# Performance work log

Measured on AMD Instinct MI355X. Metric: run time of the kernel, lower is better.

Reference implementation:

```python
import jax, jax.numpy as jnp
import numpy as np

N = 131072
D = 512        # input_dim
H = 512        # hidden_dim
E = 10         # num_experts
INIT_STD_SCALE = 0.1


def _trunc_normal(key, shape, std):
    # approximate trunc_normal_(std=std) in [-2std, 2std]
    return jnp.clip(jax.random.normal(key, shape) * std, -2.0 * std, 2.0 * std).astype(jnp.float32)


def setup_inputs() -> dict:
    key = jax.random.key(0)
    ks = jax.random.split(key, 6)
    x = jax.random.normal(ks[0], (N, D), dtype=jnp.float32)
    # router (default nn.Linear init approximated with uniform)
    lim = 1.0 / np.sqrt(D)
    Wr = jax.random.uniform(ks[1], (E, D), minval=-lim, maxval=lim, dtype=jnp.float32)
    br = jnp.zeros((E,), dtype=jnp.float32)
    # experts: trunc_normal with std = 0.1 / sqrt(fan_in), zero bias
    W1 = _trunc_normal(ks[2], (E, D, H), INIT_STD_SCALE / np.sqrt(D))   # [E, D, H]
    b1 = jnp.zeros((E, H), dtype=jnp.float32)
    W2 = _trunc_normal(ks[3], (E, H, H), INIT_STD_SCALE / np.sqrt(H))   # [E, H, H]
    b2 = jnp.zeros((E, H), dtype=jnp.float32)
    return {"x": x, "Wr": Wr, "br": br, "W1": W1, "b1": b1, "W2": W2, "b2": b2}


def reference(x, Wr, br, W1, b1, W2, b2):
    # router in fp32 (autocast disabled in original)
    logits = x.astype(jnp.float32) @ Wr.T + br          # [N, E]
    expert_ids = jnp.argmax(logits, axis=1)              # [N]
    out = jnp.zeros((x.shape[0], W2.shape[-1]), dtype=x.dtype)
    # fixed small loop over experts; dropout is identity at inference
    for e in range(W1.shape[0]):
        h = jax.nn.relu(x @ W1[e] + b1[e])                # [N, H]
        o = h @ W2[e] + b2[e]                             # [N, H]
        out = jnp.where((expert_ids == e)[:, None], o, out)
    return out, expert_ids
```

## Files before the change

kernel.cpp:

```cpp
#include <hip/hip_runtime.h>

#define N_TOK 131072
#define DIM   512
#define HID   512
#define NEXP  10

using bf16x8 = __attribute__((ext_vector_type(8))) short;
using f32x4  = __attribute__((ext_vector_type(4))) float;

__device__ __forceinline__ ushort f2bf(float f) {
    union { float f; unsigned u; } v; v.f = f;
    unsigned u = v.u;
    return (ushort)((u + 0x7FFFu + ((u >> 16) & 1u)) >> 16);
}

#define GLOAD16(g, l) __builtin_amdgcn_global_load_lds( \
    (const __attribute__((address_space(1))) void*)(g),  \
    (__attribute__((address_space(3))) void*)(l), 16, 0, 0)

__global__ __launch_bounds__(256) void router_kernel(
    const float* __restrict__ x, const float* __restrict__ Wr,
    const float* __restrict__ br, int* __restrict__ eid,
    float* __restrict__ ids_out, int* __restrict__ counts)
{
    __shared__ float wr[NEXP][DIM];
    __shared__ int lcnt[NEXP];
    int tid = threadIdx.x;
    for (int i = tid; i < NEXP * DIM / 4; i += 256)
        ((float4*)wr)[i] = ((const float4*)Wr)[i];
    if (tid < NEXP) lcnt[tid] = 0;
    __syncthreads();

    int lane  = tid & 63;
    int wave  = tid >> 6;
    int gwave = blockIdx.x * 4 + wave;
    int nwav  = gridDim.x * 4;

    for (int t = gwave; t < N_TOK; t += nwav) {
        const float4* xr = (const float4*)(x + (size_t)t * DIM);
        float4 v0 = xr[lane * 2], v1 = xr[lane * 2 + 1];
        float xf[8] = {v0.x, v0.y, v0.z, v0.w, v1.x, v1.y, v1.z, v1.w};
        float dot[NEXP];
        #pragma unroll
        for (int e = 0; e < NEXP; ++e) {
            const float* wv = &wr[e][lane * 8];
            float s = 0.f;
            #pragma unroll
            for (int j = 0; j < 8; ++j) s = fmaf(xf[j], wv[j], s);
            dot[e] = s;
        }
        #pragma unroll
        for (int off = 32; off > 0; off >>= 1) {
            #pragma unroll
            for (int e = 0; e < NEXP; ++e) dot[e] += __shfl_xor(dot[e], off, 64);
        }
        if (lane == 0) {
            int best = 0; float bv = dot[0] + br[0];
            #pragma unroll
            for (int e = 1; e < NEXP; ++e) {
                float v = dot[e] + br[e];
                if (v > bv) { bv = v; best = e; }
            }
            eid[t] = best;
            ids_out[t] = (float)best;
            atomicAdd(&lcnt[best], 1);
        }
    }
    __syncthreads();
    if (tid < NEXP) atomicAdd(&counts[tid], lcnt[tid]);
}

__global__ void offsets_kernel(const int* __restrict__ counts,
                               int* __restrict__ offsets, int* __restrict__ toff)
{
    if (threadIdx.x == 0) {
        int acc = 0, ta = 0;
        for (int e = 0; e < NEXP; ++e) {
            offsets[e] = acc; toff[e] = ta;
            acc += counts[e]; ta += (counts[e] + 63) >> 6;
        }
        offsets[NEXP] = acc; toff[NEXP] = ta;
    }
}

__global__ __launch_bounds__(256) void scatter_kernel(
    const int* __restrict__ eid, const int* __restrict__ offsets,
    int* __restrict__ cursors, int* __restrict__ perm)
{
    __shared__ int lcnt[NEXP], lbase[NEXP];
    int tid = threadIdx.x;
    if (tid < NEXP) lcnt[tid] = 0;
    __syncthreads();
    int t = blockIdx.x * 256 + tid;
    int e = 0, lpos = 0;
    if (t < N_TOK) {
        e = eid[t];
        lpos = atomicAdd(&lcnt[e], 1);
    }
    __syncthreads();
    if (tid < NEXP) lbase[tid] = atomicAdd(&cursors[tid], lcnt[tid]);
    __syncthreads();
    if (t < N_TOK) perm[offsets[e] + lbase[e] + lpos] = t;
}

__global__ __launch_bounds__(256) void wconvert_kernel(
    const float* __restrict__ W1, const float* __restrict__ W2,
    short* __restrict__ W1bT, short* __restrict__ W2bT)
{
    int mat = blockIdx.z;
    const float* src = (mat < NEXP) ? W1 + (size_t)mat * 512 * 512
                                    : W2 + (size_t)(mat - NEXP) * 512 * 512;
    short* dst = (mat < NEXP) ? W1bT + (size_t)mat * 512 * 512
                              : W2bT + (size_t)(mat - NEXP) * 512 * 512;
    __shared__ float tile[64][65];
    int r0 = blockIdx.y * 64, c0 = blockIdx.x * 64;
    int tid = threadIdx.x;
    int tr = tid >> 4, tc4 = (tid & 15) * 4;
    #pragma unroll
    for (int i = 0; i < 4; ++i) {
        float4 v = *(const float4*)(src + (size_t)(r0 + i * 16 + tr) * 512 + c0 + tc4);
        tile[i * 16 + tr][tc4 + 0] = v.x; tile[i * 16 + tr][tc4 + 1] = v.y;
        tile[i * 16 + tr][tc4 + 2] = v.z; tile[i * 16 + tr][tc4 + 3] = v.w;
    }
    __syncthreads();
    #pragma unroll
    for (int i = 0; i < 4; ++i) {
        int cc = i * 16 + tr;
        ushort4 o;
        o.x = f2bf(tile[tc4 + 0][cc]); o.y = f2bf(tile[tc4 + 1][cc]);
        o.z = f2bf(tile[tc4 + 2][cc]); o.w = f2bf(tile[tc4 + 3][cc]);
        *(ushort4*)(dst + (size_t)(c0 + cc) * 512 + r0 + tc4) = o;
    }
}

template<int LAYER>
__global__ __launch_bounds__(256, 2) void expert_gemm(
    const float* __restrict__ x, const short* __restrict__ hA,
    const short* __restrict__ WT, const float* __restrict__ bias,
    const int* __restrict__ offsets, const int* __restrict__ toff,
    const int* __restrict__ perm,
    short* __restrict__ hOut, float* __restrict__ out)
{
    int g = blockIdx.x;
    if (g >= toff[NEXP]) return;
    int e = 0;
    #pragma unroll
    for (int k = 1; k < NEXP; ++k) e += (g >= toff[k]);
    int beg = offsets[e], cnt = offsets[e + 1] - beg;
    int m0 = (g - toff[e]) * 64;

    __shared__ int toks[64];
    __shared__ short Abuf[2][64 * 32];
    __shared__ short Bbuf[2][512 * 32];

    int tid = threadIdx.x, lane = tid & 63, w = tid >> 6;
    if (tid < 64) toks[tid] = perm[beg + min(m0 + tid, cnt - 1)];
    __syncthreads();

    int srow = tid >> 2;
    int skq  = tid & 3;
    const float* asrcF = nullptr;
    const short* asrcH = nullptr;
    if (LAYER == 1) asrcF = x + (size_t)toks[srow] * DIM + skq * 8;
    else            asrcH = hA + (size_t)(beg + min(m0 + srow, cnt - 1)) * HID + skq * 8;
    const short* bsrc = WT + (size_t)e * 512 * 512 + (size_t)srow * 512 + skq * 8;

    auto stage = [&](int t, int b) {
        float4 a0, a1;
        if (LAYER == 1) {
            a0 = *(const float4*)(asrcF + t * 32);
            a1 = *(const float4*)(asrcF + t * 32 + 4);
        } else {
            GLOAD16(asrcH + t * 32, (char*)&Abuf[b][0] + w * 1024);
        }
        const short* bs = bsrc + t * 32;
        char* bl = (char*)&Bbuf[b][0] + w * 1024;
        #pragma unroll
        for (int r = 0; r < 8; ++r)
            GLOAD16(bs + (size_t)r * 64 * 512, bl + r * 4096);
        if (LAYER == 1) {
            bf16x8 ap;
            ap[0] = (short)f2bf(a0.x); ap[1] = (short)f2bf(a0.y);
            ap[2] = (short)f2bf(a0.z); ap[3] = (short)f2bf(a0.w);
            ap[4] = (short)f2bf(a1.x); ap[5] = (short)f2bf(a1.y);
            ap[6] = (short)f2bf(a1.z); ap[7] = (short)f2bf(a1.w);
            *(bf16x8*)((char*)&Abuf[b][0] + srow * 64 + skq * 16) = ap;
        }
    };

    f32x4 acc[4][8];
    #pragma unroll
    for (int i = 0; i < 4; ++i)
        #pragma unroll
        for (int j = 0; j < 8; ++j) acc[i][j] = (f32x4){0.f, 0.f, 0.f, 0.f};

    int lrow = lane & 15;
    int lk   = (lane >> 4) * 8;

    auto compute = [&](int b) {
        const short* A = &Abuf[b][0];
        const short* B = &Bbuf[b][0];
        bf16x8 af[4], bfv[8];
        #pragma unroll
        for (int i = 0; i < 4; ++i)
            af[i] = *(const bf16x8*)(A + (i * 16 + lrow) * 32 + lk);
        #pragma unroll
        for (int j = 0; j < 8; ++j)
            bfv[j] = *(const bf16x8*)(B + (w * 128 + j * 16 + lrow) * 32 + lk);
        #pragma unroll
        for (int i = 0; i < 4; ++i)
            #pragma unroll
            for (int j = 0; j < 8; ++j)
                acc[i][j] = __builtin_amdgcn_mfma_f32_16x16x32_bf16(af[i], bfv[j], acc[i][j], 0, 0, 0);
    };

    stage(0, 0);
    __syncthreads();
    #pragma unroll 1
    for (int t = 0; t < 14; t += 2) {
        stage(t + 1, 1); compute(0); __syncthreads();
        stage(t + 2, 0); compute(1); __syncthreads();
    }
    stage(15, 1); compute(0); __syncthreads();
    compute(1);

    const float* be = bias + (size_t)e * 512;
    int colb = w * 128 + lrow;
    float bv[8];
    #pragma unroll
    for (int j = 0; j < 8; ++j) bv[j] = be[colb + j * 16];

    #pragma unroll
    for (int i = 0; i < 4; ++i) {
        #pragma unroll
        for (int q = 0; q < 4; ++q) {
            int rr = i * 16 + ((lane >> 4) << 2) + q;
            if (m0 + rr < cnt) {
                if (LAYER == 1) {
                    short* hp = hOut + (size_t)(beg + m0 + rr) * HID + colb;
                    #pragma unroll
                    for (int j = 0; j < 8; ++j) {
                        float v = acc[i][j][q] + bv[j];
                        hp[j * 16] = (short)f2bf(v > 0.f ? v : 0.f);
                    }
                } else {
                    float* op = out + (size_t)toks[rr] * HID + colb;
                    #pragma unroll
                    for (int j = 0; j < 8; ++j)
                        op[j * 16] = acc[i][j][q] + bv[j];
                }
            }
        }
    }
}

extern "C" void kernel_launch(void* const* d_in, const int* in_sizes, int n_in,
                              void* d_out, int out_size, void* d_ws, size_t ws_size,
                              hipStream_t stream)
{
    const float* x  = (const float*)d_in[0];
    const float* Wr = (const float*)d_in[1];
    const float* br = (const float*)d_in[2];
    const float* W1 = (const float*)d_in[3];
    const float* b1 = (const float*)d_in[4];
    const float* W2 = (const float*)d_in[5];
    const float* b2 = (const float*)d_in[6];

    float* out     = (float*)d_out;
    float* ids_out = out + (size_t)N_TOK * HID;

    char* ws     = (char*)d_ws;
    int* counts  = (int*)ws;
    int* offsets = counts + 16;
    int* toff    = counts + 32;
    int* cursors = counts + 48;
    int* eid     = (int*)(ws + 1024);
    int* perm    = eid + N_TOK;
    short* W1bT  = (short*)(ws + 1024 + (size_t)2 * N_TOK * 4);
    short* W2bT  = W1bT + (size_t)NEXP * 512 * 512;
    short* h     = W2bT + (size_t)NEXP * 512 * 512;

    hipMemsetAsync(d_ws, 0, 1024, stream);
    router_kernel<<<2048, 256, 0, stream>>>(x, Wr, br, eid, ids_out, counts);
    wconvert_kernel<<<dim3(8, 8, 2 * NEXP), 256, 0, stream>>>(W1, W2, W1bT, W2bT);
    offsets_kernel<<<1, 64, 0, stream>>>(counts, offsets, toff);
    scatter_kernel<<<512, 256, 0, stream>>>(eid, offsets, cursors, perm);

    int ntiles = (N_TOK + 63) / 64 + NEXP;
    expert_gemm<1><<<ntiles, 256, 0, stream>>>(x, nullptr, W1bT, b1, offsets, toff, perm, h, nullptr);
    expert_gemm<2><<<ntiles, 256, 0, stream>>>(nullptr, h, W2bT, b2, offsets, toff, perm, nullptr, out);
}
```

Baseline: 434.0 us.

## Retile expert GEMM to 128x256 tiles with 8 waves and N split

Changes the grouped expert GEMM from 64-token x 512-column tiles with 4 waves to 128-token x 256-column tiles with 8 waves arranged 2x4, launching two column blocks per token tile. Each wave now holds a 64x64 accumulator instead of 64x128, which lowers register pressure and targets higher occupancy (launch bounds 512,4). The A tile is reused across more columns per weight load, but the A operand (including the layer-1 fp32 gather and bf16 conversion) is now loaded twice, once per column block. Padding waste per expert also grows with the larger row tile.

```diff
diff --git a/kernel.cpp b/kernel.cpp
--- a/kernel.cpp
+++ b/kernel.cpp
@@ -1,4 +1,5 @@
 #include <hip/hip_runtime.h>
+#include <hip/hip_bf16.h>
 
 #define N_TOK 131072
 #define DIM   512
@@ -8,10 +9,10 @@
 using bf16x8 = __attribute__((ext_vector_type(8))) short;
 using f32x4  = __attribute__((ext_vector_type(4))) float;
 
-__device__ __forceinline__ ushort f2bf(float f) {
+__device__ __forceinline__ short f2bf(float f) {
     union { float f; unsigned u; } v; v.f = f;
     unsigned u = v.u;
-    return (ushort)((u + 0x7FFFu + ((u >> 16) & 1u)) >> 16);
+    return (short)((u + 0x7FFFu + ((u >> 16) & 1u)) >> 16);
 }
 
 #define GLOAD16(g, l) __builtin_amdgcn_global_load_lds( \
@@ -77,7 +78,7 @@
         int acc = 0, ta = 0;
         for (int e = 0; e < NEXP; ++e) {
             offsets[e] = acc; toff[e] = ta;
-            acc += counts[e]; ta += (counts[e] + 63) >> 6;
+            acc += counts[e]; ta += (counts[e] + 127) >> 7;
         }
         offsets[NEXP] = acc; toff[NEXP] = ta;
     }
@@ -127,14 +128,14 @@
     for (int i = 0; i < 4; ++i) {
         int cc = i * 16 + tr;
         ushort4 o;
-        o.x = f2bf(tile[tc4 + 0][cc]); o.y = f2bf(tile[tc4 + 1][cc]);
-        o.z = f2bf(tile[tc4 + 2][cc]); o.w = f2bf(tile[tc4 + 3][cc]);
+        o.x = (ushort)f2bf(tile[tc4 + 0][cc]); o.y = (ushort)f2bf(tile[tc4 + 1][cc]);
+        o.z = (ushort)f2bf(tile[tc4 + 2][cc]); o.w = (ushort)f2bf(tile[tc4 + 3][cc]);
         *(ushort4*)(dst + (size_t)(c0 + cc) * 512 + r0 + tc4) = o;
     }
 }
 
 template<int LAYER>
-__global__ __launch_bounds__(256, 2) void expert_gemm(
+__global__ __launch_bounds__(512, 4) void expert_gemm(
     const float* __restrict__ x, const short* __restrict__ hA,
     const short* __restrict__ WT, const float* __restrict__ bias,
     const int* __restrict__ offsets, const int* __restrict__ toff,
@@ -147,70 +148,65 @@
     #pragma unroll
     for (int k = 1; k < NEXP; ++k) e += (g >= toff[k]);
     int beg = offsets[e], cnt = offsets[e + 1] - beg;
-    int m0 = (g - toff[e]) * 64;
-
-    __shared__ int toks[64];
-    __shared__ short Abuf[2][64 * 32];
-    __shared__ short Bbuf[2][512 * 32];
+    int m0 = (g - toff[e]) * 128;
+    int nb = blockIdx.y * 256;
+
+    __shared__ int toks[128];
+    __shared__ short Abuf[2][128 * 32];
+    __shared__ short Bbuf[2][256 * 32];
 
     int tid = threadIdx.x, lane = tid & 63, w = tid >> 6;
-    if (tid < 64) toks[tid] = perm[beg + min(m0 + tid, cnt - 1)];
-    __syncthreads();
-
-    int srow = tid >> 2;
-    int skq  = tid & 3;
-    const float* asrcF = nullptr;
-    const short* asrcH = nullptr;
-    if (LAYER == 1) asrcF = x + (size_t)toks[srow] * DIM + skq * 8;
-    else            asrcH = hA + (size_t)(beg + min(m0 + srow, cnt - 1)) * HID + skq * 8;
-    const short* bsrc = WT + (size_t)e * 512 * 512 + (size_t)srow * 512 + skq * 8;
+    if (tid < 128) toks[tid] = perm[beg + min(m0 + tid, cnt - 1)];
+    __syncthreads();
+
+    int arow = tid >> 2;
+    int kq   = tid & 3;
+    const float* xr   = nullptr;
+    const short* ha   = nullptr;
+    if (LAYER == 1) xr = x + (size_t)toks[arow] * DIM + kq * 8;
+    else            ha = hA + (size_t)(beg + min(m0 + arow, cnt - 1)) * HID + kq * 8;
+    const short* bp = WT + (size_t)e * 512 * 512 + (size_t)(nb + (tid >> 2)) * 512 + kq * 8;
 
     auto stage = [&](int t, int b) {
-        float4 a0, a1;
+        char* bl = (char*)&Bbuf[b][0] + w * 1024;
+        GLOAD16(bp + t * 32,         bl);
+        GLOAD16(bp + t * 32 + 65536, bl + 8192);
         if (LAYER == 1) {
-            a0 = *(const float4*)(asrcF + t * 32);
-            a1 = *(const float4*)(asrcF + t * 32 + 4);
+            float4 a0 = *(const float4*)(xr + t * 32);
+            float4 a1 = *(const float4*)(xr + t * 32 + 4);
+            bf16x8 p;
+            p[0] = f2bf(a0.x); p[1] = f2bf(a0.y); p[2] = f2bf(a0.z); p[3] = f2bf(a0.w);
+            p[4] = f2bf(a1.x); p[5] = f2bf(a1.y); p[6] = f2bf(a1.z); p[7] = f2bf(a1.w);
+            *(bf16x8*)((char*)&Abuf[b][0] + tid * 16) = p;
         } else {
-            GLOAD16(asrcH + t * 32, (char*)&Abuf[b][0] + w * 1024);
-        }
-        const short* bs = bsrc + t * 32;
-        char* bl = (char*)&Bbuf[b][0] + w * 1024;
-        #pragma unroll
-        for (int r = 0; r < 8; ++r)
-            GLOAD16(bs + (size_t)r * 64 * 512, bl + r * 4096);
-        if (LAYER == 1) {
-            bf16x8 ap;
-            ap[0] = (short)f2bf(a0.x); ap[1] = (short)f2bf(a0.y);
-            ap[2] = (short)f2bf(a0.z); ap[3] = (short)f2bf(a0.w);
-            ap[4] = (short)f2bf(a1.x); ap[5] = (short)f2bf(a1.y);
-            ap[6] = (short)f2bf(a1.z); ap[7] = (short)f2bf(a1.w);
-            *(bf16x8*)((char*)&Abuf[b][0] + srow * 64 + skq * 16) = ap;
+            GLOAD16(ha + t * 32, (char*)&Abuf[b][0] + w * 1024);
         }
     };
 
-    f32x4 acc[4][8];
+    f32x4 acc[4][4];
     #pragma unroll
     for (int i = 0; i < 4; ++i)
         #pragma unroll
-        for (int j = 0; j < 8; ++j) acc[i][j] = (f32x4){0.f, 0.f, 0.f, 0.f};
-
+        for (int j = 0; j < 4; ++j) acc[i][j] = (f32x4){0.f, 0.f, 0.f, 0.f};
+
+    int wr = w >> 2, wc = w & 3;
     int lrow = lane & 15;
     int lk   = (lane >> 4) * 8;
 
     auto compute = [&](int b) {
         const short* A = &Abuf[b][0];
         const short* B = &Bbuf[b][0];
-        bf16x8 af[4], bfv[8];
+        bf16x8 af[4], bfv[4];
         #pragma unroll
         for (int i = 0; i < 4; ++i)
-            af[i] = *(const bf16x8*)(A + (i * 16 + lrow) * 32 + lk);
-        #pragma unroll
-        for (int j = 0; j < 8; ++j)
-            bfv[j] = *(const bf16x8*)(B + (w * 128 + j * 16 + lrow) * 32 + lk);
+            af[i] = *(const bf16x8*)(A + (wr * 64 + i * 16 + lrow) * 32 + lk);
+        #pragma unroll
+        for (int j = 0; j < 4; ++j)
+            bfv[j] = *(const bf16x8*)(B + (wc * 64 + j * 16 + lrow) * 32 + lk);
         #pragma unroll
         for (int i = 0; i < 4; ++i)
             #pragma unroll
-            for (int j = 0; j < 8; ++j)
+            for (int j = 0; j < 4; ++j)
                 acc[i][j] = __builtin_amdgcn_mfma_f32_16x16x32_bf16(af[i], bfv[j], acc[i][j], 0, 0, 0);
     };
 
@@ -225,28 +221,28 @@
     compute(1);
 
     const float* be = bias + (size_t)e * 512;
-    int colb = w * 128 + lrow;
-    float bv[8];
-    #pragma unroll
-    for (int j = 0; j < 8; ++j) bv[j] = be[colb + j * 16];
+    int colb = nb + wc * 64 + lrow;
+    float bv[4];
+    #pragma unroll
+    for (int j = 0; j < 4; ++j) bv[j] = be[colb + j * 16];
 
     #pragma unroll
     for (int i = 0; i < 4; ++i) {
         #pragma unroll
         for (int q = 0; q < 4; ++q) {
-            int rr = i * 16 + ((lane >> 4) << 2) + q;
+            int rr = wr * 64 + i * 16 + ((lane >> 4) << 2) + q;
             if (m0 + rr < cnt) {
                 if (LAYER == 1) {
                     short* hp = hOut + (size_t)(beg + m0 + rr) * HID + colb;
                     #pragma unroll
-                    for (int j = 0; j < 8; ++j) {
+                    for (int j = 0; j < 4; ++j) {
                         float v = acc[i][j][q] + bv[j];
-                        hp[j * 16] = (short)f2bf(v > 0.f ? v : 0.f);
+                        hp[j * 16] = f2bf(v > 0.f ? v : 0.f);
                     }
                 } else {
                     float* op = out + (size_t)toks[rr] * HID + colb;
                     #pragma unroll
-                    for (int j = 0; j < 8; ++j)
+                    for (int j = 0; j < 4; ++j)
                         op[j * 16] = acc[i][j][q] + bv[j];
                 }
             }
@@ -286,7 +282,7 @@
     offsets_kernel<<<1, 64, 0, stream>>>(counts, offsets, toff);
     scatter_kernel<<<512, 256, 0, stream>>>(eid, offsets, cursors, perm);
 
-    int ntiles = (N_TOK + 63) / 64 + NEXP;
-    expert_gemm<1><<<ntiles, 256, 0, stream>>>(x, nullptr, W1bT, b1, offsets, toff, perm, h, nullptr);
-    expert_gemm<2><<<ntiles, 256, 0, stream>>>(nullptr, h, W2bT, b2, offsets, toff, perm, nullptr, out);
-}
+    int ntiles = (N_TOK + 127) / 128 + NEXP;
+    expert_gemm<1><<<dim3(ntiles, 2), 512, 0, stream>>>(x, nullptr, W1bT, b1, offsets, toff, perm, h, nullptr);
+    expert_gemm<2><<<dim3(ntiles, 2), 512, 0, stream>>>(nullptr, h, W2bT, b2, offsets, toff, perm, nullptr, out);
+}
```

After: 434.4 us. About the same (+0.1%).
